# Kernel tuning notes

Measured on AMD Instinct MI355X. Metric: run time of the kernel, lower is better.

## Reference

```python
import jax, jax.numpy as jnp
import numpy as np


def setup_inputs() -> dict:
    key = jax.random.key(0)
    k1, k2 = jax.random.split(key)
    x = jax.random.normal(k1, (32, 64, 64, 64), dtype=jnp.float32)
    codebook = jax.random.normal(k2, (1024, 64), dtype=jnp.float32)
    return {"x": x, "codebook": codebook}


def reference(x, codebook):
    # x: (B, D, H, W)  codebook: (K, D)
    B, D = x.shape[0], x.shape[1]
    spatial = x.shape[2:]
    flat = x.reshape(B, D, -1).transpose(0, 2, 1)  # (B, N, D)
    dot = jnp.einsum("bnd,kd->bnk", flat, codebook)
    cb_norm = jnp.sum(codebook * codebook, axis=-1)  # (K,)
    indices = jnp.argmin(cb_norm[None, None, :] - 2.0 * dot, axis=-1)  # (B, N)
    quantized = codebook[indices]  # (B, N, D) gather
    out = quantized.transpose(0, 2, 1).reshape(x.shape)
    return out, indices.reshape((B,) + spatial)
```

## Files before the change

kernel.cpp:

```cpp
#include <hip/hip_runtime.h>


typedef _Float16 f16x8 __attribute__((ext_vector_type(8)));
typedef float    f32x4 __attribute__((ext_vector_type(4)));

#define VQ_D    64
#define VQ_HW   4096
#define VQ_NPOS 131072
#define SC      2048.0f
#define EPS_Q   24
#define WS_CBN  65536
#define WS_CNQ  66560
#define WS_CBT  67584
#define WS_CNT  133120
#define WS_LIST 133124

__global__ __launch_bounds__(256)
void vq_prep(const float* __restrict__ cb, float* __restrict__ ws)
{
    const int tid = threadIdx.x;
    const int blk = blockIdx.x;
    if (blk < 64) {
        const int it   = blk * 256 + tid;
        const int ct   = it >> 8;
        const int s    = (it >> 6) & 3;
        const int lane = it & 63;
        const int ks   = s & 1, isR = s >> 1;
        const int n    = ct * 16 + (lane & 15);
        const int k0   = ks * 32 + (lane >> 4) * 8;
        const float* src = cb + n * 64 + k0;
        f16x8 o;
        #pragma unroll
        for (int j = 0; j < 8; ++j) {
            const float b = src[j];
            const _Float16 bh = (_Float16)b;
            o[j] = isR ? (_Float16)((b - (float)bh) * (-2.0f * SC))
                       : (_Float16)(-2.0f * (float)bh);
        }
        ((f16x8*)ws)[it] = o;
    } else if (blk < 128) {
        const int it = (blk - 64) * 256 + tid;
        const int k = it >> 4, j4 = it & 15;
        ((float4*)(ws + WS_CBT))[j4 * 1024 + k] = ((const float4*)cb)[it];
    } else {
        const int k = (blk - 128) * 256 + tid;
        const float4* row = (const float4*)(cb + k * 64);
        float a0 = 0.f, a1 = 0.f, a2 = 0.f, a3 = 0.f;
        #pragma unroll
        for (int j = 0; j < 16; ++j) {
            const float4 c = row[j];
            a0 = fmaf(c.x, c.x, a0); a1 = fmaf(c.y, c.y, a1);
            a2 = fmaf(c.z, c.z, a2); a3 = fmaf(c.w, c.w, a3);
        }
        const float cn = (a0 + a1) + (a2 + a3);
        ws[WS_CBN + k] = cn;
        ws[WS_CNQ + k] = cn * 2048.0f;
        if (k == 0) ((int*)ws)[WS_CNT] = 0;
    }
}

#define GLOAD_LDS(GP, LP)                                                     \
    __builtin_amdgcn_global_load_lds(                                         \
        (const __attribute__((address_space(1))) unsigned int*)(GP),          \
        (__attribute__((address_space(3))) unsigned int*)(LP), 16, 0, 0)

#define STAGE2(CK, BOFF)                                                      \
    {                                                                         \
        const char* gs_ = (const char*)ws + (size_t)(CK) * 8192               \
                          + wv * 2048 + lane * 16;                            \
        char* ld_ = (char*)bbuf + (BOFF) + wv * 2048;                         \
        GLOAD_LDS(gs_, ld_);                                                  \
        GLOAD_LDS(gs_ + 1024, ld_ + 1024);                                    \
    }

#define CT_BODY(BOFF, CI, CTG)                                                \
    {                                                                         \
        const f16x8 B0 = *(const f16x8*)(lp + (BOFF) + (CI) * 4096);          \
        const f16x8 B1 = *(const f16x8*)(lp + (BOFF) + (CI) * 4096 + 1024);   \
        const f16x8 R0 = *(const f16x8*)(lp + (BOFF) + (CI) * 4096 + 2048);   \
        const f16x8 R1 = *(const f16x8*)(lp + (BOFF) + (CI) * 4096 + 3072);   \
        const float cvq = cnq_lds[(CTG) * 16 + m];                            \
        const f32x4 Ci = {cvq, cvq, cvq, cvq};                                \
        __builtin_amdgcn_s_setprio(1);                                        \
        f32x4 pa0 = __builtin_amdgcn_mfma_f32_16x16x32_f16(Ak[0][0], B0, Ci,    0,0,0); \
        f32x4 pb0 = __builtin_amdgcn_mfma_f32_16x16x32_f16(Ak[0][1], B1, zero4, 0,0,0); \
        f32x4 pa1 = __builtin_amdgcn_mfma_f32_16x16x32_f16(Ak[1][0], B0, Ci,    0,0,0); \
        f32x4 pb1 = __builtin_amdgcn_mfma_f32_16x16x32_f16(Ak[1][1], B1, zero4, 0,0,0); \
        pa0 = __builtin_amdgcn_mfma_f32_16x16x32_f16(Ah[0][0], R0, pa0, 0,0,0); \
        pb0 = __builtin_amdgcn_mfma_f32_16x16x32_f16(Ah[0][1], R1, pb0, 0,0,0); \
        pa1 = __builtin_amdgcn_mfma_f32_16x16x32_f16(Ah[1][0], R0, pa1, 0,0,0); \
        pb1 = __builtin_amdgcn_mfma_f32_16x16x32_f16(Ah[1][1], R1, pb1, 0,0,0); \
        pa0 = __builtin_amdgcn_mfma_f32_16x16x32_f16(Ra[0][0], B0, pa0, 0,0,0); \
        pb0 = __builtin_amdgcn_mfma_f32_16x16x32_f16(Ra[0][1], B1, pb0, 0,0,0); \
        pa1 = __builtin_amdgcn_mfma_f32_16x16x32_f16(Ra[1][0], B0, pa1, 0,0,0); \
        pb1 = __builtin_amdgcn_mfma_f32_16x16x32_f16(Ra[1][1], B1, pb1, 0,0,0); \
        __builtin_amdgcn_s_setprio(0);                                        \
        const int cbase_ = (CTG) * 16 + m;                                    \
        _Pragma("unroll")                                                     \
        for (int r = 0; r < 4; ++r) {                                         \
            const float q0_ = pa0[r] + pb0[r];                                \
            const int k0_ = ((int)q0_ << 10) | cbase_;                        \
            int m0_;                                                          \
            asm("v_med3_i32 %0, %1, %2, %3"                                   \
                : "=v"(m0_) : "v"(k0_), "v"(d1[0][r]), "v"(d2[0][r]));        \
            d2[0][r] = m0_;                                                   \
            d1[0][r] = (k0_ < d1[0][r]) ? k0_ : d1[0][r];                     \
            const float q1_ = pa1[r] + pb1[r];                                \
            const int k1_ = ((int)q1_ << 10) | cbase_;                        \
            int m1_;                                                          \
            asm("v_med3_i32 %0, %1, %2, %3"                                   \
                : "=v"(m1_) : "v"(k1_), "v"(d1[1][r]), "v"(d2[1][r]));        \
            d2[1][r] = m1_;                                                   \
            d1[1][r] = (k1_ < d1[1][r]) ? k1_ : d1[1][r];                     \
        }                                                                     \
        __builtin_amdgcn_sched_barrier(0x100);    \
    }

#define ITER_T(VMSTR, DOSTAGE, T)                                             \
    {                                                                         \
        asm volatile("s_waitcnt " VMSTR ::: "memory");                        \
        __builtin_amdgcn_s_barrier();                                         \
        if (DOSTAGE) STAGE2((T) + 3, (((T) + 3) & 3) * 8192)                  \
        const int base_ = ((T) & 3) * 8192;                                   \
        CT_BODY(base_, 0, (T) * 2)                                            \
        CT_BODY(base_, 1, (T) * 2 + 1)                                        \
    }

__global__ __launch_bounds__(256, 4)
void vq_main(const float* __restrict__ x,
             const float* __restrict__ cb,
             float* __restrict__ ws,
             float* __restrict__ out,
             float* __restrict__ idx_out)
{
    __shared__ f16x8 bbuf[4 * 512];
    __shared__ float cnq_lds[1024];
    __shared__ int   sk[128];
    __shared__ int   smg[128];

    const int tid  = threadIdx.x;
    const int lane = tid & 63;
    const int wv   = tid >> 6;
    const int m    = lane & 15;
    const int q    = lane >> 4;

    const int p0 = blockIdx.x * 128;
    const int b  = p0 >> 12;
    const int n0 = p0 & (VQ_HW - 1);
    const float* xw = x + (size_t)b * (VQ_D * VQ_HW) + n0 + wv * 32;

    STAGE2(0, 0)
    STAGE2(1, 8192)
    STAGE2(2, 16384)

    ((float4*)cnq_lds)[tid] = ((const float4*)(ws + WS_CNQ))[tid];

    f16x8 Ah[2][2], Ak[2][2], Ra[2][2];
    #pragma unroll
    for (int tl = 0; tl < 2; ++tl)
        #pragma unroll
        for (int ks = 0; ks < 2; ++ks) {
            f16x8 h8, k8, r8;
            #pragma unroll
            for (int j = 0; j < 8; ++j) {
                const float v = xw[(size_t)(ks * 32 + q * 8 + j) * VQ_HW + tl * 16 + m];
                const _Float16 vh = (_Float16)v;
                h8[j] = vh;
                k8[j] = (_Float16)((float)vh * 2048.0f);
                r8[j] = (_Float16)((v - (float)vh) * SC);
            }
            Ah[tl][ks] = h8; Ak[tl][ks] = k8; Ra[tl][ks] = r8;
        }

    int d1[2][4], d2[2][4];
    #pragma unroll
    for (int tl = 0; tl < 2; ++tl)
        #pragma unroll
        for (int r = 0; r < 4; ++r) { d1[tl][r] = 0x7FFFFFFF; d2[tl][r] = 0x7FFFFFFF; }

    const f32x4 zero4 = {0.f, 0.f, 0.f, 0.f};
    const char* lp = (const char*)bbuf + lane * 16;

    __syncthreads();

    for (int t = 0; t < 29; ++t)
        ITER_T("vmcnt(4)", 1, t)
    ITER_T("vmcnt(4)", 0, 29)
    ITER_T("vmcnt(2)", 0, 30)
    ITER_T("vmcnt(0)", 0, 31)

    #pragma unroll
    for (int off = 1; off < 16; off <<= 1)
        #pragma unroll
        for (int tl = 0; tl < 2; ++tl)
            #pragma unroll
            for (int r = 0; r < 4; ++r) {
                const int od1 = __shfl_xor(d1[tl][r], off, 64);
                const int od2 = __shfl_xor(d2[tl][r], off, 64);
                const int mx  = (d1[tl][r] > od1) ? d1[tl][r] : od1;
                const int mn2 = (d2[tl][r] < od2) ? d2[tl][r] : od2;
                d2[tl][r] = (mx < mn2) ? mx : mn2;
                d1[tl][r] = (d1[tl][r] < od1) ? d1[tl][r] : od1;
            }

    if (m == 0) {
        #pragma unroll
        for (int tl = 0; tl < 2; ++tl)
            #pragma unroll
            for (int r = 0; r < 4; ++r) {
                const int li = wv * 32 + tl * 16 + q * 4 + r;
                sk[li]  = d1[tl][r] & 1023;
                smg[li] = (d2[tl][r] >> 10) - (d1[tl][r] >> 10);
            }
    }
    __syncthreads();

    const int pos  = tid & 127;
    const int half = tid >> 7;
    const int bk   = sk[pos];
    if (half == 0) {
        idx_out[p0 + pos] = (float)bk;
        if (smg[pos] < EPS_Q) {
            const int slot = atomicAdd((int*)ws + WS_CNT, 1);
            ((int*)ws)[WS_LIST + slot] = p0 + pos;
        }
    }
    const float4* cr = (const float4*)(cb + (size_t)bk * VQ_D) + half * 8;
    float* ob = out + (size_t)b * (VQ_D * VQ_HW) + (size_t)(half * 32) * VQ_HW + n0 + pos;
    #pragma unroll
    for (int d4 = 0; d4 < 8; ++d4) {
        const float4 v = cr[d4];
        ob[(size_t)(d4 * 4 + 0) * VQ_HW] = v.x;
        ob[(size_t)(d4 * 4 + 1) * VQ_HW] = v.y;
        ob[(size_t)(d4 * 4 + 2) * VQ_HW] = v.z;
        ob[(size_t)(d4 * 4 + 3) * VQ_HW] = v.w;
    }
}

__global__ __launch_bounds__(64)
void vq_rescan(const float* __restrict__ x,
               const float* __restrict__ cb,
               const float* __restrict__ ws,
               float* __restrict__ out,
               float* __restrict__ idx_out)
{
    __shared__ float xs[VQ_D];
    const int lane = threadIdx.x;
    const int cnt  = ((const int*)ws)[WS_CNT];
    const int* list = (const int*)ws + WS_LIST;
    const float*  cnb  = ws + WS_CBN;
    const float4* cbT4 = (const float4*)(ws + WS_CBT);

    for (int i = blockIdx.x; i < cnt; i += gridDim.x) {
        const int p = list[i];
        const int b = p >> 12, n = p & (VQ_HW - 1);
        xs[lane] = x[(size_t)b * (VQ_D * VQ_HW) + (size_t)lane * VQ_HW + n];
        __syncthreads();
        float4 xr[16];
        #pragma unroll
        for (int j = 0; j < 16; ++j) xr[j] = ((const float4*)xs)[j];

        float bd = 3.4e38f; int bk = 0;
        #pragma unroll 4
        for (int t = 0; t < 16; ++t) {
            const int code = t * 64 + lane;
            float a0 = 0.f, a1 = 0.f, a2 = 0.f, a3 = 0.f;
            #pragma unroll
            for (int j4 = 0; j4 < 16; ++j4) {
                const float4 c = cbT4[j4 * 1024 + code];
                a0 = fmaf(xr[j4].x, c.x, a0); a1 = fmaf(xr[j4].y, c.y, a1);
                a2 = fmaf(xr[j4].z, c.z, a2); a3 = fmaf(xr[j4].w, c.w, a3);
            }
            const float dist = fmaf(-2.0f, (a0 + a1) + (a2 + a3), cnb[code]);
            if (dist < bd) { bd = dist; bk = code; }
        }
        #pragma unroll
        for (int off = 1; off < 64; off <<= 1) {
            const float od = __shfl_xor(bd, off, 64);
            const int   ok = __shfl_xor(bk, off, 64);
            if (od < bd || (od == bd && ok < bk)) { bd = od; bk = ok; }
        }
        out[(size_t)b * (VQ_D * VQ_HW) + (size_t)lane * VQ_HW + n] = cb[(size_t)bk * VQ_D + lane];
        if (lane == 0) idx_out[p] = (float)bk;
        __syncthreads();
    }
}

extern "C" void kernel_launch(void* const* d_in, const int* in_sizes, int n_in,
                              void* d_out, int out_size, void* d_ws, size_t ws_size,
                              hipStream_t stream) {
    const float* x  = (const float*)d_in[0];
    const float* cb = (const float*)d_in[1];
    float* out = (float*)d_out;
    float* idx = out + (size_t)VQ_NPOS * VQ_D;
    float* ws  = (float*)d_ws;

    vq_prep  <<<dim3(132),  dim3(256), 0, stream>>>(cb, ws);
    vq_main  <<<dim3(1024), dim3(256), 0, stream>>>(x, cb, ws, out, idx);
    vq_rescan<<<dim3(1024), dim3(64),  0, stream>>>(x, cb, ws, out, idx);
}
```

Before: 158.5 us.

## Double positions per wave to reuse each staged codebook tile across more rows

Each wave now handles 64 positions (four 16-row tiles) instead of 32, so each block covers 256 positions and the grid halves to 512 blocks. Every codebook tile staged into LDS is reused for twice as many MFMAs, halving total codebook LDS traffic and global staging per position. The cost is doubled A-fragment and running-min register state per thread, with launch bounds lowered to 2 blocks per CU, which reduces occupancy and may cause spilling or weaker latency hiding. With 512 blocks on 256 CUs there is less tail flexibility.

```diff
diff --git a/kernel.cpp b/kernel.cpp
--- a/kernel.cpp
+++ b/kernel.cpp
@@ -81,38 +81,37 @@
         const f16x8 R1 = *(const f16x8*)(lp + (BOFF) + (CI) * 4096 + 3072);   \
         const float cvq = cnq_lds[(CTG) * 16 + m];                            \
         const f32x4 Ci = {cvq, cvq, cvq, cvq};                                \
+        f32x4 pa[4], pb[4];                                                   \
         __builtin_amdgcn_s_setprio(1);                                        \
-        f32x4 pa0 = __builtin_amdgcn_mfma_f32_16x16x32_f16(Ak[0][0], B0, Ci,    0,0,0); \
-        f32x4 pb0 = __builtin_amdgcn_mfma_f32_16x16x32_f16(Ak[0][1], B1, zero4, 0,0,0); \
-        f32x4 pa1 = __builtin_amdgcn_mfma_f32_16x16x32_f16(Ak[1][0], B0, Ci,    0,0,0); \
-        f32x4 pb1 = __builtin_amdgcn_mfma_f32_16x16x32_f16(Ak[1][1], B1, zero4, 0,0,0); \
-        pa0 = __builtin_amdgcn_mfma_f32_16x16x32_f16(Ah[0][0], R0, pa0, 0,0,0); \
-        pb0 = __builtin_amdgcn_mfma_f32_16x16x32_f16(Ah[0][1], R1, pb0, 0,0,0); \
-        pa1 = __builtin_amdgcn_mfma_f32_16x16x32_f16(Ah[1][0], R0, pa1, 0,0,0); \
-        pb1 = __builtin_amdgcn_mfma_f32_16x16x32_f16(Ah[1][1], R1, pb1, 0,0,0); \
-        pa0 = __builtin_amdgcn_mfma_f32_16x16x32_f16(Ra[0][0], B0, pa0, 0,0,0); \
-        pb0 = __builtin_amdgcn_mfma_f32_16x16x32_f16(Ra[0][1], B1, pb0, 0,0,0); \
-        pa1 = __builtin_amdgcn_mfma_f32_16x16x32_f16(Ra[1][0], B0, pa1, 0,0,0); \
-        pb1 = __builtin_amdgcn_mfma_f32_16x16x32_f16(Ra[1][1], B1, pb1, 0,0,0); \
+        _Pragma("unroll")                                                     \
+        for (int tl = 0; tl < 4; ++tl) {                                      \
+            pa[tl] = __builtin_amdgcn_mfma_f32_16x16x32_f16(Ak[tl][0], B0, Ci,    0,0,0); \
+            pb[tl] = __builtin_amdgcn_mfma_f32_16x16x32_f16(Ak[tl][1], B1, zero4, 0,0,0); \
+        }                                                                     \
+        _Pragma("unroll")                                                     \
+        for (int tl = 0; tl < 4; ++tl) {                                      \
+            pa[tl] = __builtin_amdgcn_mfma_f32_16x16x32_f16(Ah[tl][0], R0, pa[tl], 0,0,0); \
+            pb[tl] = __builtin_amdgcn_mfma_f32_16x16x32_f16(Ah[tl][1], R1, pb[tl], 0,0,0); \
+        }                                                                     \
+        _Pragma("unroll")                                                     \
+        for (int tl = 0; tl < 4; ++tl) {                                      \
+            pa[tl] = __builtin_amdgcn_mfma_f32_16x16x32_f16(Ra[tl][0], B0, pa[tl], 0,0,0); \
+            pb[tl] = __builtin_amdgcn_mfma_f32_16x16x32_f16(Ra[tl][1], B1, pb[tl], 0,0,0); \
+        }                                                                     \
         __builtin_amdgcn_s_setprio(0);                                        \
         const int cbase_ = (CTG) * 16 + m;                                    \
         _Pragma("unroll")                                                     \
-        for (int r = 0; r < 4; ++r) {                                         \
-            const float q0_ = pa0[r] + pb0[r];                                \
-            const int k0_ = ((int)q0_ << 10) | cbase_;                        \
-            int m0_;                                                          \
-            asm("v_med3_i32 %0, %1, %2, %3"                                   \
-                : "=v"(m0_) : "v"(k0_), "v"(d1[0][r]), "v"(d2[0][r]));        \
-            d2[0][r] = m0_;                                                   \
-            d1[0][r] = (k0_ < d1[0][r]) ? k0_ : d1[0][r];                     \
-            const float q1_ = pa1[r] + pb1[r];                                \
-            const int k1_ = ((int)q1_ << 10) | cbase_;                        \
-            int m1_;                                                          \
-            asm("v_med3_i32 %0, %1, %2, %3"                                   \
-                : "=v"(m1_) : "v"(k1_), "v"(d1[1][r]), "v"(d2[1][r]));        \
-            d2[1][r] = m1_;                                                   \
-            d1[1][r] = (k1_ < d1[1][r]) ? k1_ : d1[1][r];                     \
-        }                                                                     \
+        for (int tl = 0; tl < 4; ++tl)                                        \
+            _Pragma("unroll")                                                 \
+            for (int r = 0; r < 4; ++r) {                                     \
+                const float q_ = pa[tl][r] + pb[tl][r];                       \
+                const int k_ = ((int)q_ << 10) | cbase_;                      \
+                int md_;                                                      \
+                asm("v_med3_i32 %0, %1, %2, %3"                               \
+                    : "=v"(md_) : "v"(k_), "v"(d1[tl][r]), "v"(d2[tl][r]));   \
+                d2[tl][r] = md_;                                              \
+                d1[tl][r] = (k_ < d1[tl][r]) ? k_ : d1[tl][r];                \
+            }                                                                 \
         __builtin_amdgcn_sched_barrier(0x100);    \
     }
 
@@ -126,7 +125,7 @@
         CT_BODY(base_, 1, (T) * 2 + 1)                                        \
     }
 
-__global__ __launch_bounds__(256, 4)
+__global__ __launch_bounds__(256, 2)
 void vq_main(const float* __restrict__ x,
              const float* __restrict__ cb,
              float* __restrict__ ws,
@@ -135,8 +134,8 @@
 {
     __shared__ f16x8 bbuf[4 * 512];
     __shared__ float cnq_lds[1024];
-    __shared__ int   sk[128];
-    __shared__ int   smg[128];
+    __shared__ int   sk[256];
+    __shared__ int   smg[256];
 
     const int tid  = threadIdx.x;
     const int lane = tid & 63;
@@ -144,10 +143,10 @@
     const int m    = lane & 15;
     const int q    = lane >> 4;
 
-    const int p0 = blockIdx.x * 128;
+    const int p0 = blockIdx.x * 256;
     const int b  = p0 >> 12;
     const int n0 = p0 & (VQ_HW - 1);
-    const float* xw = x + (size_t)b * (VQ_D * VQ_HW) + n0 + wv * 32;
+    const float* xw = x + (size_t)b * (VQ_D * VQ_HW) + n0 + wv * 64;
 
     STAGE2(0, 0)
     STAGE2(1, 8192)
@@ -155,9 +154,9 @@
 
     ((float4*)cnq_lds)[tid] = ((const float4*)(ws + WS_CNQ))[tid];
 
-    f16x8 Ah[2][2], Ak[2][2], Ra[2][2];
-    #pragma unroll
-    for (int tl = 0; tl < 2; ++tl)
+    f16x8 Ah[4][2], Ak[4][2], Ra[4][2];
+    #pragma unroll
+    for (int tl = 0; tl < 4; ++tl)
         #pragma unroll
         for (int ks = 0; ks < 2; ++ks) {
             f16x8 h8, k8, r8;
@@ -172,9 +171,9 @@
             Ah[tl][ks] = h8; Ak[tl][ks] = k8; Ra[tl][ks] = r8;
         }
 
-    int d1[2][4], d2[2][4];
-    #pragma unroll
-    for (int tl = 0; tl < 2; ++tl)
+    int d1[4][4], d2[4][4];
+    #pragma unroll
+    for (int tl = 0; tl < 4; ++tl)
         #pragma unroll
         for (int r = 0; r < 4; ++r) { d1[tl][r] = 0x7FFFFFFF; d2[tl][r] = 0x7FFFFFFF; }
 
@@ -192,7 +191,7 @@
     #pragma unroll
     for (int off = 1; off < 16; off <<= 1)
         #pragma unroll
-        for (int tl = 0; tl < 2; ++tl)
+        for (int tl = 0; tl < 4; ++tl)
             #pragma unroll
             for (int r = 0; r < 4; ++r) {
                 const int od1 = __shfl_xor(d1[tl][r], off, 64);
@@ -205,30 +204,26 @@
 
     if (m == 0) {
         #pragma unroll
-        for (int tl = 0; tl < 2; ++tl)
+        for (int tl = 0; tl < 4; ++tl)
             #pragma unroll
             for (int r = 0; r < 4; ++r) {
-                const int li = wv * 32 + tl * 16 + q * 4 + r;
+                const int li = wv * 64 + tl * 16 + q * 4 + r;
                 sk[li]  = d1[tl][r] & 1023;
                 smg[li] = (d2[tl][r] >> 10) - (d1[tl][r] >> 10);
             }
     }
     __syncthreads();
 
-    const int pos  = tid & 127;
-    const int half = tid >> 7;
-    const int bk   = sk[pos];
-    if (half == 0) {
-        idx_out[p0 + pos] = (float)bk;
-        if (smg[pos] < EPS_Q) {
-            const int slot = atomicAdd((int*)ws + WS_CNT, 1);
-            ((int*)ws)[WS_LIST + slot] = p0 + pos;
-        }
-    }
-    const float4* cr = (const float4*)(cb + (size_t)bk * VQ_D) + half * 8;
-    float* ob = out + (size_t)b * (VQ_D * VQ_HW) + (size_t)(half * 32) * VQ_HW + n0 + pos;
-    #pragma unroll
-    for (int d4 = 0; d4 < 8; ++d4) {
+    const int bk = sk[tid];
+    idx_out[p0 + tid] = (float)bk;
+    if (smg[tid] < EPS_Q) {
+        const int slot = atomicAdd((int*)ws + WS_CNT, 1);
+        ((int*)ws)[WS_LIST + slot] = p0 + tid;
+    }
+    const float4* cr = (const float4*)(cb + (size_t)bk * VQ_D);
+    float* ob = out + (size_t)b * (VQ_D * VQ_HW) + n0 + tid;
+    #pragma unroll
+    for (int d4 = 0; d4 < 16; ++d4) {
         const float4 v = cr[d4];
         ob[(size_t)(d4 * 4 + 0) * VQ_HW] = v.x;
         ob[(size_t)(d4 * 4 + 1) * VQ_HW] = v.y;
@@ -296,6 +291,6 @@
     float* ws  = (float*)d_ws;
 
     vq_prep  <<<dim3(132),  dim3(256), 0, stream>>>(cb, ws);
-    vq_main  <<<dim3(1024), dim3(256), 0, stream>>>(x, cb, ws, out, idx);
+    vq_main  <<<dim3(512),  dim3(256), 0, stream>>>(x, cb, ws, out, idx);
     vq_rescan<<<dim3(1024), dim3(64),  0, stream>>>(x, cb, ws, out, idx);
 }
```

After: 155.4 us. 1.02x faster.

## Switch distance GEMM from 16x16x32 to 32x32x16 MFMA tiles

Applied to the files above, without the earlier changes.

Replaces the per-iteration pair of 16x16 codebook tiles with a single 32x32x16 MFMA tile. The A operand now covers 32 positions per wave with 4 K-slices, and the codebook prep layout is reordered to match. Argmin tracking moves to 16 accumulators per lane, with a 32-lane shuffle reduction. This aims for higher MFMA throughput and fewer LDS reads per FLOP, but raises register pressure, so launch bounds drop to 2 blocks per SM and the sched_barrier is removed.

```diff
diff --git a/kernel.cpp b/kernel.cpp
--- a/kernel.cpp
+++ b/kernel.cpp
@@ -1,8 +1,8 @@
 #include <hip/hip_runtime.h>
 
 
-typedef _Float16 f16x8 __attribute__((ext_vector_type(8)));
-typedef float    f32x4 __attribute__((ext_vector_type(4)));
+typedef _Float16 f16x8  __attribute__((ext_vector_type(8)));
+typedef float    f32x16 __attribute__((ext_vector_type(16)));
 
 #define VQ_D    64
 #define VQ_HW   4096
@@ -22,20 +22,20 @@
     const int blk = blockIdx.x;
     if (blk < 64) {
         const int it   = blk * 256 + tid;
-        const int ct   = it >> 8;
-        const int s    = (it >> 6) & 3;
+        const int ct32 = it >> 9;
+        const int s    = (it >> 8) & 1;
+        const int kq   = (it >> 6) & 3;
         const int lane = it & 63;
-        const int ks   = s & 1, isR = s >> 1;
-        const int n    = ct * 16 + (lane & 15);
-        const int k0   = ks * 32 + (lane >> 4) * 8;
+        const int n    = ct32 * 32 + (lane & 31);
+        const int k0   = kq * 16 + (lane >> 5) * 8;
         const float* src = cb + n * 64 + k0;
         f16x8 o;
         #pragma unroll
         for (int j = 0; j < 8; ++j) {
             const float b = src[j];
             const _Float16 bh = (_Float16)b;
-            o[j] = isR ? (_Float16)((b - (float)bh) * (-2.0f * SC))
-                       : (_Float16)(-2.0f * (float)bh);
+            o[j] = s ? (_Float16)((b - (float)bh) * (-2.0f * SC))
+                     : (_Float16)(-2.0f * (float)bh);
         }
         ((f16x8*)ws)[it] = o;
     } else if (blk < 128) {
@@ -73,47 +73,45 @@
         GLOAD_LDS(gs_ + 1024, ld_ + 1024);                                    \
     }
 
-#define CT_BODY(BOFF, CI, CTG)                                                \
+#define CT32_BODY(BOFF, CT32)                                                 \
     {                                                                         \
-        const f16x8 B0 = *(const f16x8*)(lp + (BOFF) + (CI) * 4096);          \
-        const f16x8 B1 = *(const f16x8*)(lp + (BOFF) + (CI) * 4096 + 1024);   \
-        const f16x8 R0 = *(const f16x8*)(lp + (BOFF) + (CI) * 4096 + 2048);   \
-        const f16x8 R1 = *(const f16x8*)(lp + (BOFF) + (CI) * 4096 + 3072);   \
-        const float cvq = cnq_lds[(CTG) * 16 + m];                            \
-        const f32x4 Ci = {cvq, cvq, cvq, cvq};                                \
+        const f16x8 B0 = *(const f16x8*)(lp + (BOFF));                        \
+        const f16x8 B1 = *(const f16x8*)(lp + (BOFF) + 1024);                 \
+        const f16x8 B2 = *(const f16x8*)(lp + (BOFF) + 2048);                 \
+        const f16x8 B3 = *(const f16x8*)(lp + (BOFF) + 3072);                 \
+        const f16x8 R0 = *(const f16x8*)(lp + (BOFF) + 4096);                 \
+        const f16x8 R1 = *(const f16x8*)(lp + (BOFF) + 5120);                 \
+        const f16x8 R2 = *(const f16x8*)(lp + (BOFF) + 6144);                 \
+        const f16x8 R3 = *(const f16x8*)(lp + (BOFF) + 7168);                 \
+        const float cvq = cnq_lds[(CT32) * 32 + (lane & 31)];                 \
+        f32x16 Ci;                                                            \
+        _Pragma("unroll")                                                     \
+        for (int r = 0; r < 16; ++r) Ci[r] = cvq;                             \
         __builtin_amdgcn_s_setprio(1);                                        \
-        f32x4 pa0 = __builtin_amdgcn_mfma_f32_16x16x32_f16(Ak[0][0], B0, Ci,    0,0,0); \
-        f32x4 pb0 = __builtin_amdgcn_mfma_f32_16x16x32_f16(Ak[0][1], B1, zero4, 0,0,0); \
-        f32x4 pa1 = __builtin_amdgcn_mfma_f32_16x16x32_f16(Ak[1][0], B0, Ci,    0,0,0); \
-        f32x4 pb1 = __builtin_amdgcn_mfma_f32_16x16x32_f16(Ak[1][1], B1, zero4, 0,0,0); \
-        pa0 = __builtin_amdgcn_mfma_f32_16x16x32_f16(Ah[0][0], R0, pa0, 0,0,0); \
-        pb0 = __builtin_amdgcn_mfma_f32_16x16x32_f16(Ah[0][1], R1, pb0, 0,0,0); \
-        pa1 = __builtin_amdgcn_mfma_f32_16x16x32_f16(Ah[1][0], R0, pa1, 0,0,0); \
-        pb1 = __builtin_amdgcn_mfma_f32_16x16x32_f16(Ah[1][1], R1, pb1, 0,0,0); \
-        pa0 = __builtin_amdgcn_mfma_f32_16x16x32_f16(Ra[0][0], B0, pa0, 0,0,0); \
-        pb0 = __builtin_amdgcn_mfma_f32_16x16x32_f16(Ra[0][1], B1, pb0, 0,0,0); \
-        pa1 = __builtin_amdgcn_mfma_f32_16x16x32_f16(Ra[1][0], B0, pa1, 0,0,0); \
-        pb1 = __builtin_amdgcn_mfma_f32_16x16x32_f16(Ra[1][1], B1, pb1, 0,0,0); \
+        f32x16 pa = __builtin_amdgcn_mfma_f32_32x32x16_f16(Ak[0], B0, Ci,     0,0,0); \
+        f32x16 pb = __builtin_amdgcn_mfma_f32_32x32x16_f16(Ah[0], R0, zero16, 0,0,0); \
+        f32x16 pc = __builtin_amdgcn_mfma_f32_32x32x16_f16(Ra[0], B0, zero16, 0,0,0); \
+        pa = __builtin_amdgcn_mfma_f32_32x32x16_f16(Ak[1], B1, pa, 0,0,0);    \
+        pb = __builtin_amdgcn_mfma_f32_32x32x16_f16(Ah[1], R1, pb, 0,0,0);    \
+        pc = __builtin_amdgcn_mfma_f32_32x32x16_f16(Ra[1], B1, pc, 0,0,0);    \
+        pa = __builtin_amdgcn_mfma_f32_32x32x16_f16(Ak[2], B2, pa, 0,0,0);    \
+        pb = __builtin_amdgcn_mfma_f32_32x32x16_f16(Ah[2], R2, pb, 0,0,0);    \
+        pc = __builtin_amdgcn_mfma_f32_32x32x16_f16(Ra[2], B2, pc, 0,0,0);    \
+        pa = __builtin_amdgcn_mfma_f32_32x32x16_f16(Ak[3], B3, pa, 0,0,0);    \
+        pb = __builtin_amdgcn_mfma_f32_32x32x16_f16(Ah[3], R3, pb, 0,0,0);    \
+        pc = __builtin_amdgcn_mfma_f32_32x32x16_f16(Ra[3], B3, pc, 0,0,0);    \
         __builtin_amdgcn_s_setprio(0);                                        \
-        const int cbase_ = (CTG) * 16 + m;                                    \
+        const int cbase_ = (CT32) * 32 + (lane & 31);                         \
         _Pragma("unroll")                                                     \
-        for (int r = 0; r < 4; ++r) {                                         \
-            const float q0_ = pa0[r] + pb0[r];                                \
-            const int k0_ = ((int)q0_ << 10) | cbase_;                        \
-            int m0_;                                                          \
+        for (int r = 0; r < 16; ++r) {                                        \
+            const float q_ = (pa[r] + pb[r]) + pc[r];                         \
+            const int k_ = ((int)q_ << 10) | cbase_;                          \
+            int md_;                                                          \
             asm("v_med3_i32 %0, %1, %2, %3"                                   \
-                : "=v"(m0_) : "v"(k0_), "v"(d1[0][r]), "v"(d2[0][r]));        \
-            d2[0][r] = m0_;                                                   \
-            d1[0][r] = (k0_ < d1[0][r]) ? k0_ : d1[0][r];                     \
-            const float q1_ = pa1[r] + pb1[r];                                \
-            const int k1_ = ((int)q1_ << 10) | cbase_;                        \
-            int m1_;                                                          \
-            asm("v_med3_i32 %0, %1, %2, %3"                                   \
-                : "=v"(m1_) : "v"(k1_), "v"(d1[1][r]), "v"(d2[1][r]));        \
-            d2[1][r] = m1_;                                                   \
-            d1[1][r] = (k1_ < d1[1][r]) ? k1_ : d1[1][r];                     \
+                : "=v"(md_) : "v"(k_), "v"(d1[r]), "v"(d2[r]));               \
+            d2[r] = md_;                                                      \
+            d1[r] = (k_ < d1[r]) ? k_ : d1[r];                                \
         }                                                                     \
-        __builtin_amdgcn_sched_barrier(0x100);    \
     }
 
 #define ITER_T(VMSTR, DOSTAGE, T)                                             \
@@ -121,12 +119,10 @@
         asm volatile("s_waitcnt " VMSTR ::: "memory");                        \
         __builtin_amdgcn_s_barrier();                                         \
         if (DOSTAGE) STAGE2((T) + 3, (((T) + 3) & 3) * 8192)                  \
-        const int base_ = ((T) & 3) * 8192;                                   \
-        CT_BODY(base_, 0, (T) * 2)                                            \
-        CT_BODY(base_, 1, (T) * 2 + 1)                                        \
-    }
-
-__global__ __launch_bounds__(256, 4)
+        CT32_BODY(((T) & 3) * 8192, T)                                        \
+    }
+
+__global__ __launch_bounds__(256, 2)
 void vq_main(const float* __restrict__ x,
              const float* __restrict__ cb,
              float* __restrict__ ws,
@@ -141,8 +137,6 @@
     const int tid  = threadIdx.x;
     const int lane = tid & 63;
     const int wv   = tid >> 6;
-    const int m    = lane & 15;
-    const int q    = lane >> 4;
 
     const int p0 = blockIdx.x * 128;
     const int b  = p0 >> 12;
@@ -155,30 +149,29 @@
 
     ((float4*)cnq_lds)[tid] = ((const float4*)(ws + WS_CNQ))[tid];
 
-    f16x8 Ah[2][2], Ak[2][2], Ra[2][2];
-    #pragma unroll
-    for (int tl = 0; tl < 2; ++tl)
-        #pragma unroll
-        for (int ks = 0; ks < 2; ++ks) {
-            f16x8 h8, k8, r8;
-            #pragma unroll
-            for (int j = 0; j < 8; ++j) {
-                const float v = xw[(size_t)(ks * 32 + q * 8 + j) * VQ_HW + tl * 16 + m];
-                const _Float16 vh = (_Float16)v;
-                h8[j] = vh;
-                k8[j] = (_Float16)((float)vh * 2048.0f);
-                r8[j] = (_Float16)((v - (float)vh) * SC);
-            }
-            Ah[tl][ks] = h8; Ak[tl][ks] = k8; Ra[tl][ks] = r8;
-        }
-
-    int d1[2][4], d2[2][4];
-    #pragma unroll
-    for (int tl = 0; tl < 2; ++tl)
-        #pragma unroll
-        for (int r = 0; r < 4; ++r) { d1[tl][r] = 0x7FFFFFFF; d2[tl][r] = 0x7FFFFFFF; }
-
-    const f32x4 zero4 = {0.f, 0.f, 0.f, 0.f};
+    f16x8 Ah[4], Ak[4], Ra[4];
+    #pragma unroll
+    for (int kq = 0; kq < 4; ++kq) {
+        f16x8 h8, k8, r8;
+        #pragma unroll
+        for (int j = 0; j < 8; ++j) {
+            const int k = kq * 16 + (lane >> 5) * 8 + j;
+            const float v = xw[(size_t)k * VQ_HW + (lane & 31)];
+            const _Float16 vh = (_Float16)v;
+            h8[j] = vh;
+            k8[j] = (_Float16)((float)vh * 2048.0f);
+            r8[j] = (_Float16)((v - (float)vh) * SC);
+        }
+        Ah[kq] = h8; Ak[kq] = k8; Ra[kq] = r8;
+    }
+
+    int d1[16], d2[16];
+    #pragma unroll
+    for (int r = 0; r < 16; ++r) { d1[r] = 0x7FFFFFFF; d2[r] = 0x7FFFFFFF; }
+
+    f32x16 zero16;
+    #pragma unroll
+    for (int r = 0; r < 16; ++r) zero16[r] = 0.0f;
     const char* lp = (const char*)bbuf + lane * 16;
 
     __syncthreads();
@@ -190,28 +183,25 @@
     ITER_T("vmcnt(0)", 0, 31)
 
     #pragma unroll
-    for (int off = 1; off < 16; off <<= 1)
-        #pragma unroll
-        for (int tl = 0; tl < 2; ++tl)
-            #pragma unroll
-            for (int r = 0; r < 4; ++r) {
-                const int od1 = __shfl_xor(d1[tl][r], off, 64);
-                const int od2 = __shfl_xor(d2[tl][r], off, 64);
-                const int mx  = (d1[tl][r] > od1) ? d1[tl][r] : od1;
-                const int mn2 = (d2[tl][r] < od2) ? d2[tl][r] : od2;
-                d2[tl][r] = (mx < mn2) ? mx : mn2;
-                d1[tl][r] = (d1[tl][r] < od1) ? d1[tl][r] : od1;
-            }
-
-    if (m == 0) {
-        #pragma unroll
-        for (int tl = 0; tl < 2; ++tl)
-            #pragma unroll
-            for (int r = 0; r < 4; ++r) {
-                const int li = wv * 32 + tl * 16 + q * 4 + r;
-                sk[li]  = d1[tl][r] & 1023;
-                smg[li] = (d2[tl][r] >> 10) - (d1[tl][r] >> 10);
-            }
+    for (int off = 1; off < 32; off <<= 1)
+        #pragma unroll
+        for (int r = 0; r < 16; ++r) {
+            const int od1 = __shfl_xor(d1[r], off, 64);
+            const int od2 = __shfl_xor(d2[r], off, 64);
+            const int mx  = (d1[r] > od1) ? d1[r] : od1;
+            const int mn2 = (d2[r] < od2) ? d2[r] : od2;
+            d2[r] = (mx < mn2) ? mx : mn2;
+            d1[r] = (d1[r] < od1) ? d1[r] : od1;
+        }
+
+    if ((lane & 31) == 0) {
+        #pragma unroll
+        for (int r = 0; r < 16; ++r) {
+            const int row = (r & 3) + 8 * (r >> 2) + 4 * (lane >> 5);
+            const int li  = wv * 32 + row;
+            sk[li]  = d1[r] & 1023;
+            smg[li] = (d2[r] >> 10) - (d1[r] >> 10);
+        }
     }
     __syncthreads();
 
```

New measurement: 175.1 us. +10.4%, slower.
